# Performance work log

Measured on AMD Instinct MI355X. Metric: run time of the kernel, lower is better.

Reference implementation:

```python
import jax, jax.numpy as jnp
import numpy as np

COMMIT_WEIGHT = 0.25


def setup_inputs() -> dict:
    key = jax.random.key(0)
    k1, k2 = jax.random.split(key)
    B, D, T, K = 8, 512, 2048, 8192
    x = jax.random.normal(k1, (B, D, T), dtype=jnp.float32)
    codebook = jax.random.normal(k2, (K, D), dtype=jnp.float32)
    return {"x": x, "codebook": codebook}


def reference(x, codebook):
    # x: [B, D, T] channels-first; VQ operates on [B, T, D]
    xt = jnp.transpose(x, (0, 2, 1))  # [B, T, D]
    x2 = jnp.sum(xt * xt, axis=-1, keepdims=True)          # [B, T, 1]
    e2 = jnp.sum(codebook * codebook, axis=-1)             # [K]
    xe = jnp.einsum('btd,kd->btk', xt, codebook)           # [B, T, K] (dominant GEMM)
    dists = x2 - 2.0 * xe + e2                             # [B, T, K]
    indices = jnp.argmin(dists, axis=-1)                   # [B, T] int
    quantized = codebook[indices]                          # [B, T, D] gather
    # commitment loss: ||sg(q) - x||^2 mean
    commit_loss = COMMIT_WEIGHT * jnp.mean(
        (jax.lax.stop_gradient(quantized) - xt) ** 2)
    # straight-through estimator
    quantized = xt + jax.lax.stop_gradient(quantized - xt)
    quantized = jnp.transpose(quantized, (0, 2, 1))        # back to [B, D, T]
    return quantized, indices, commit_loss
```

## Files before the change

kernel.cpp:

```cpp
#include <hip/hip_runtime.h>
#include <cstdint>
#include <cstddef>

#define B_   8
#define D_   512
#define T_   2048
#define K_   8192
#define BT_  (B_ * T_)
#define NQ_  ((size_t)B_ * D_ * T_)

typedef _Float16 f16x8 __attribute__((ext_vector_type(8)));
typedef _Float16 f16x4 __attribute__((ext_vector_type(4)));
typedef float    f32x4 __attribute__((ext_vector_type(4)));
typedef unsigned long long u64;
typedef unsigned int u32;

#define WS_SLOTS_OFF    0
#define WS_FIDX_OFF     393216
#define WS_PART_OFF     458752
#define WS_E2_OFF       460800
#define WS_XH_OFF       524288
#define WS_XL_OFF       (WS_XH_OFF + 16777216)
#define WS_CH_OFF       (WS_XL_OFF + 16777216)
#define WS_NEEDED       ((size_t)WS_CH_OFF + 8388608)

__device__ __forceinline__ void gload_lds16(const void* g, void* l) {
    __builtin_amdgcn_global_load_lds(
        (const __attribute__((address_space(1))) void*)g,
        (__attribute__((address_space(3))) void*)l, 16, 0, 0);
}

__device__ __forceinline__ u32 fkey(float f) {
    u32 u = __float_as_uint(f);
    u ^= (u32)((int)u >> 31) | 0x80000000u;
    return u;
}
__device__ __forceinline__ u64 umin64(u64 a, u64 b) { return a < b ? a : b; }
__device__ __forceinline__ u64 umax64(u64 a, u64 b) { return a > b ? a : b; }

__global__ __launch_bounds__(256) void k_e2(const float* __restrict__ cb,
                                            float* __restrict__ e2) {
    int k = blockIdx.x * 256 + threadIdx.x;
    const float4* row = (const float4*)(cb + (size_t)k * D_);
    float s = 0.f;
#pragma unroll 4
    for (int i = 0; i < D_ / 4; ++i) {
        float4 v = row[i];
        s = fmaf(v.x, v.x, s); s = fmaf(v.y, v.y, s);
        s = fmaf(v.z, v.z, s); s = fmaf(v.w, v.w, s);
    }
    e2[k] = s;
}

__global__ __launch_bounds__(256) void k_splitcb(const float* __restrict__ cb,
                                                 _Float16* __restrict__ ch) {
    size_t i = ((size_t)blockIdx.x * 256 + threadIdx.x) * 4;
    float4 v = *(const float4*)(cb + i);
    f16x4 h;
    h[0] = (_Float16)v.x; h[1] = (_Float16)v.y;
    h[2] = (_Float16)v.z; h[3] = (_Float16)v.w;
    *(f16x4*)(ch + i) = h;
}

__global__ __launch_bounds__(256) void k_splitx(const float* __restrict__ x,
                                                _Float16* __restrict__ xh,
                                                _Float16* __restrict__ xl) {
    int b  = blockIdx.z;
    int d0 = blockIdx.y * 64;
    int t0 = blockIdx.x * 64;
    int dl = threadIdx.x & 63;
    int tq = threadIdx.x >> 6;
    const float* px = x + ((size_t)b * D_ + (d0 + dl)) * T_ + t0;
#pragma unroll 4
    for (int i = 0; i < 16; ++i) {
        int t = tq * 16 + i;
        float v = px[t];
        _Float16 h = (_Float16)v;
        float lo = v - (float)h;
        _Float16 l = (_Float16)lo;
        size_t row = (size_t)b * T_ + t0 + t;
        xh[row * D_ + d0 + dl] = h;
        xl[row * D_ + d0 + dl] = l;
    }
}

__global__ __launch_bounds__(256, 2)
void k_hi_argmin(const _Float16* __restrict__ xh, const _Float16* __restrict__ ch,
                 const float* __restrict__ e2, u64* __restrict__ slots) {
    __shared__ char smem[65536];
    __shared__ u32 stop[128][2][2];
    __shared__ float e2s[1024];

    const int tid = threadIdx.x;
    const int xcd = blockIdx.x & 7;
    const int bi  = blockIdx.x >> 3;
    const int m_  = bi >> 3;
    const int nblk = bi & 7;
    const int mbase  = (xcd * 16 + m_) * 128;
    const int nstart = nblk * 1024;

    const int lane = tid & 63;
    const int wid  = tid >> 6;
    const int wr = wid >> 1, wc = wid & 1;
    const int lr = lane & 15, lg = lane >> 4;

    {
        u32* p = (u32*)stop;
        p[tid] = ~0u; p[tid + 256] = ~0u;
        *(float4*)&e2s[tid * 4] = *(const float4*)&e2[nstart + tid * 4];
    }
    __syncthreads();

    const bool isA = wid < 2;
    const int half = wid & 1;
    const int srow8 = lane >> 3;
    const int sswz = ((lane & 7) ^ srow8) * 16;
    const char* gs0 = isA
        ? (const char*)xh + (size_t)(mbase  + half * 64 + srow8) * 1024 + sswz
        : (const char*)ch + (size_t)(nstart + half * 64 + srow8) * 1024 + sswz;
    const int ldsbase = (isA ? 0 : 16384) + half * 8192;

#define STAGE(bufi, g) do {                                                  \
        char* lb_ = smem + (bufi) * 32768 + ldsbase;                         \
        const char* gs_ = gs0 + (isA ? 0 : (size_t)((g) >> 3) * 131072)      \
                          + ((g) & 7) * 128;                                 \
        _Pragma("unroll")                                                    \
        for (int i_ = 0; i_ < 8; ++i_)                                       \
            gload_lds16(gs_ + (size_t)i_ * 8192, lb_ + i_ * 1024);           \
    } while (0)

    const int s7 = lr & 7;
    const int aoff0 = (wr * 64 + lr) * 128 + ((lg ^ s7) * 16);
    const int boff0 = 16384 + (wc * 64 + lr) * 128 + ((lg ^ s7) * 16);

    u32 top2a[16], top2b[16];
#pragma unroll
    for (int s = 0; s < 16; ++s) { top2a[s] = ~0u; top2b[s] = ~0u; }

    f32x4 acc[4][4];
#pragma unroll
    for (int m = 0; m < 4; ++m)
#pragma unroll
        for (int n = 0; n < 4; ++n)
            acc[m][n] = (f32x4){0.f, 0.f, 0.f, 0.f};

    auto epilogue = [&](int ns) {
        float e2v[4];
#pragma unroll
        for (int n = 0; n < 4; ++n)
            e2v[n] = 0.5f * e2s[ns * 128 + wc * 64 + n * 16 + lr];
        const u32 base10 = ((u32)ns << 7) | ((u32)wc << 6) | (u32)lr;
#pragma unroll
        for (int m = 0; m < 4; ++m) {
#pragma unroll
            for (int j = 0; j < 4; ++j) {
                const int s = m * 4 + j;
                u32 t1 = top2a[s], t2 = top2b[s];
#pragma unroll
                for (int n = 0; n < 4; ++n) {
                    float d = fmaxf(e2v[n] - acc[m][n][j], 1.0f);
                    u32 p = (__float_as_uint(d) & 0xFFFFFC00u) | (base10 + ((u32)n << 4));
                    u32 mx = t1 > p ? t1 : p;
                    t1 = t1 < p ? t1 : p;
                    t2 = t2 < mx ? t2 : mx;
                }
                top2a[s] = t1; top2b[s] = t2;
            }
        }
#pragma unroll
        for (int m = 0; m < 4; ++m)
#pragma unroll
            for (int n = 0; n < 4; ++n)
                acc[m][n] = (f32x4){0.f, 0.f, 0.f, 0.f};
    };

    STAGE(0, 0);
    int cur = 0;

#pragma unroll 1
    for (int t = 0; t < 64; ++t) {
        if (t < 63) {
            STAGE(cur ^ 1, t + 1);
            asm volatile("s_waitcnt vmcnt(8)" ::: "memory");
        } else {
            asm volatile("s_waitcnt vmcnt(0)" ::: "memory");
        }
        __builtin_amdgcn_s_barrier();
        __builtin_amdgcn_sched_barrier(0);

        const char* base = smem + cur * 32768;
        f16x8 a0, a1, a2, a3, b0, b1, b2, b3;
        f16x8 c0, c1, c2, c3, d0, d1, d2, d3;
        a0 = *(const f16x8*)(base + aoff0);
        a1 = *(const f16x8*)(base + aoff0 + 2048);
        a2 = *(const f16x8*)(base + aoff0 + 4096);
        a3 = *(const f16x8*)(base + aoff0 + 6144);
        b0 = *(const f16x8*)(base + boff0);
        b1 = *(const f16x8*)(base + boff0 + 2048);
        b2 = *(const f16x8*)(base + boff0 + 4096);
        b3 = *(const f16x8*)(base + boff0 + 6144);
        c0 = *(const f16x8*)(base + (aoff0 ^ 64));
        c1 = *(const f16x8*)(base + ((aoff0 + 2048) ^ 64));
        c2 = *(const f16x8*)(base + ((aoff0 + 4096) ^ 64));
        c3 = *(const f16x8*)(base + ((aoff0 + 6144) ^ 64));
        d0 = *(const f16x8*)(base + (boff0 ^ 64));
        d1 = *(const f16x8*)(base + ((boff0 + 2048) ^ 64));
        d2 = *(const f16x8*)(base + ((boff0 + 4096) ^ 64));
        d3 = *(const f16x8*)(base + ((boff0 + 6144) ^ 64));

        __builtin_amdgcn_s_setprio(1);
        acc[0][0] = __builtin_amdgcn_mfma_f32_16x16x32_f16(a0, b0, acc[0][0], 0, 0, 0);
        acc[0][1] = __builtin_amdgcn_mfma_f32_16x16x32_f16(a0, b1, acc[0][1], 0, 0, 0);
        acc[0][2] = __builtin_amdgcn_mfma_f32_16x16x32_f16(a0, b2, acc[0][2], 0, 0, 0);
        acc[0][3] = __builtin_amdgcn_mfma_f32_16x16x32_f16(a0, b3, acc[0][3], 0, 0, 0);
        acc[1][0] = __builtin_amdgcn_mfma_f32_16x16x32_f16(a1, b0, acc[1][0], 0, 0, 0);
        acc[1][1] = __builtin_amdgcn_mfma_f32_16x16x32_f16(a1, b1, acc[1][1], 0, 0, 0);
        acc[1][2] = __builtin_amdgcn_mfma_f32_16x16x32_f16(a1, b2, acc[1][2], 0, 0, 0);
        acc[1][3] = __builtin_amdgcn_mfma_f32_16x16x32_f16(a1, b3, acc[1][3], 0, 0, 0);
        acc[2][0] = __builtin_amdgcn_mfma_f32_16x16x32_f16(a2, b0, acc[2][0], 0, 0, 0);
        acc[2][1] = __builtin_amdgcn_mfma_f32_16x16x32_f16(a2, b1, acc[2][1], 0, 0, 0);
        acc[2][2] = __builtin_amdgcn_mfma_f32_16x16x32_f16(a2, b2, acc[2][2], 0, 0, 0);
        acc[2][3] = __builtin_amdgcn_mfma_f32_16x16x32_f16(a2, b3, acc[2][3], 0, 0, 0);
        acc[3][0] = __builtin_amdgcn_mfma_f32_16x16x32_f16(a3, b0, acc[3][0], 0, 0, 0);
        acc[3][1] = __builtin_amdgcn_mfma_f32_16x16x32_f16(a3, b1, acc[3][1], 0, 0, 0);
        acc[3][2] = __builtin_amdgcn_mfma_f32_16x16x32_f16(a3, b2, acc[3][2], 0, 0, 0);
        acc[3][3] = __builtin_amdgcn_mfma_f32_16x16x32_f16(a3, b3, acc[3][3], 0, 0, 0);
        acc[0][0] = __builtin_amdgcn_mfma_f32_16x16x32_f16(c0, d0, acc[0][0], 0, 0, 0);
        acc[0][1] = __builtin_amdgcn_mfma_f32_16x16x32_f16(c0, d1, acc[0][1], 0, 0, 0);
        acc[0][2] = __builtin_amdgcn_mfma_f32_16x16x32_f16(c0, d2, acc[0][2], 0, 0, 0);
        acc[0][3] = __builtin_amdgcn_mfma_f32_16x16x32_f16(c0, d3, acc[0][3], 0, 0, 0);
        acc[1][0] = __builtin_amdgcn_mfma_f32_16x16x32_f16(c1, d0, acc[1][0], 0, 0, 0);
        acc[1][1] = __builtin_amdgcn_mfma_f32_16x16x32_f16(c1, d1, acc[1][1], 0, 0, 0);
        acc[1][2] = __builtin_amdgcn_mfma_f32_16x16x32_f16(c1, d2, acc[1][2], 0, 0, 0);
        acc[1][3] = __builtin_amdgcn_mfma_f32_16x16x32_f16(c1, d3, acc[1][3], 0, 0, 0);
        acc[2][0] = __builtin_amdgcn_mfma_f32_16x16x32_f16(c2, d0, acc[2][0], 0, 0, 0);
        acc[2][1] = __builtin_amdgcn_mfma_f32_16x16x32_f16(c2, d1, acc[2][1], 0, 0, 0);
        acc[2][2] = __builtin_amdgcn_mfma_f32_16x16x32_f16(c2, d2, acc[2][2], 0, 0, 0);
        acc[2][3] = __builtin_amdgcn_mfma_f32_16x16x32_f16(c2, d3, acc[2][3], 0, 0, 0);
        acc[3][0] = __builtin_amdgcn_mfma_f32_16x16x32_f16(c3, d0, acc[3][0], 0, 0, 0);
        acc[3][1] = __builtin_amdgcn_mfma_f32_16x16x32_f16(c3, d1, acc[3][1], 0, 0, 0);
        acc[3][2] = __builtin_amdgcn_mfma_f32_16x16x32_f16(c3, d2, acc[3][2], 0, 0, 0);
        acc[3][3] = __builtin_amdgcn_mfma_f32_16x16x32_f16(c3, d3, acc[3][3], 0, 0, 0);
        __builtin_amdgcn_s_setprio(0);

        __builtin_amdgcn_sched_barrier(0);
        __builtin_amdgcn_s_barrier();
        cur ^= 1;
        if ((t & 7) == 7) epilogue(t >> 3);
    }
#undef STAGE

#pragma unroll
    for (int m = 0; m < 4; ++m) {
#pragma unroll
        for (int j = 0; j < 4; ++j) {
            const int s = m * 4 + j;
            u32 t1 = top2a[s], t2 = top2b[s];
#pragma unroll
            for (int st = 1; st < 16; st <<= 1) {
                u32 o1 = __shfl_xor(t1, st);
                u32 o2 = __shfl_xor(t2, st);
                u32 mx = t1 > o1 ? t1 : o1;
                u32 sel = t1 < o1 ? t2 : o2;
                u32 n2 = mx < sel ? mx : sel;
                t1 = t1 < o1 ? t1 : o1;
                t2 = t2 < n2 ? t2 : n2;
            }
            if (lr == 0) {
                int ql = wr * 64 + m * 16 + lg * 4 + j;
                stop[ql][wc][0] = t1; stop[ql][wc][1] = t2;
            }
        }
    }

    __syncthreads();
    if (tid < 128) {
        u32 a1 = stop[tid][0][0], a2 = stop[tid][0][1];
        u32 b1 = stop[tid][1][0], b2 = stop[tid][1][1];
        u32 f1 = a1 < b1 ? a1 : b1;
        u32 mx = a1 > b1 ? a1 : b1;
        u32 sel = a1 < b1 ? a2 : b2;
        u32 f2 = mx < sel ? mx : sel;
        int q = mbase + tid;
        u64 p1 = ((u64)(f1 & 0xFFFFFC00u) << 32) | (u32)(nstart + (f1 & 0x3FFu));
        u64 p2 = ((u64)(f2 & 0xFFFFFC00u) << 32) | (u32)(nstart + (f2 & 0x3FFu));
        u64* As = slots + q;
        u64* Bs = slots + BT_ + q;
        u64* Cs = slots + 2 * BT_ + q;
        u64 old = atomicMin(As, p1);
        u64 v = umax64(old, p1);
        old = atomicMin(Bs, v);
        u64 v2 = umax64(old, v);
        atomicMin(Cs, v2);
        old = atomicMin(Bs, p2);
        v = umax64(old, p2);
        atomicMin(Cs, v);
    }
}

__global__ __launch_bounds__(256)
void k_rescore(const _Float16* __restrict__ xh, const _Float16* __restrict__ xl,
               const float* __restrict__ cb, const float* __restrict__ e2,
               const u64* __restrict__ slots,
               u32* __restrict__ final_idx, float* __restrict__ out_idx) {
    const int wid = threadIdx.x >> 6, lane = threadIdx.x & 63;
    const int q = blockIdx.x * 4 + wid;
    u64 a = slots[q], b = slots[BT_ + q], c = slots[2 * BT_ + q];
    u32 i1 = (u32)a, i2 = (u32)b, i3 = (u32)c;
    float d1 = __uint_as_float((u32)(a >> 32));
    float d2 = __uint_as_float((u32)(b >> 32));
    u32 win = i1;
    if (!(d2 - d1 > 0.75f)) {
        float xr[8];
        f16x8 hv = *(const f16x8*)(xh + (size_t)q * D_ + lane * 8);
        f16x8 lv = *(const f16x8*)(xl + (size_t)q * D_ + lane * 8);
#pragma unroll
        for (int i = 0; i < 8; ++i) xr[i] = (float)hv[i] + (float)lv[i];
        u32 idxs[3] = {i1, i2, i3};
        float key[3];
#pragma unroll 1
        for (int cnd = 0; cnd < 3; ++cnd) {
            const float4* cr = (const float4*)(cb + (size_t)idxs[cnd] * D_ + lane * 8);
            float4 c0 = cr[0], c1 = cr[1];
            float s = xr[0] * c0.x;
            s = fmaf(xr[1], c0.y, s); s = fmaf(xr[2], c0.z, s); s = fmaf(xr[3], c0.w, s);
            s = fmaf(xr[4], c1.x, s); s = fmaf(xr[5], c1.y, s);
            s = fmaf(xr[6], c1.z, s); s = fmaf(xr[7], c1.w, s);
#pragma unroll
            for (int st = 1; st < 64; st <<= 1) s += __shfl_xor(s, st);
            key[cnd] = e2[idxs[cnd]] - 2.f * s;
        }
        float bk = key[0]; win = idxs[0];
#pragma unroll
        for (int cnd = 1; cnd < 3; ++cnd) {
            if (key[cnd] < bk || (key[cnd] == bk && idxs[cnd] < win)) {
                bk = key[cnd]; win = idxs[cnd];
            }
        }
    }
    if (lane == 0) { final_idx[q] = win; out_idx[q] = (float)win; }
}

#define MB 64
#define NB 64
#define KC 32
#define FNSPLIT 2
#define KPER (K_ / FNSPLIT)
__global__ __launch_bounds__(256, 2)
void k_argmin_f32(const float* __restrict__ x, const float* __restrict__ cb,
                  const float* __restrict__ e2, u64* __restrict__ slots) {
    __shared__ float xs[KC][MB + 4];
    __shared__ float es[KC][NB + 4];
    __shared__ u64 red[MB];
    const int tid = threadIdx.x;
    const int tx = tid & 15, ty = tid >> 4;
    const int rowtile = blockIdx.x;
    const int b = rowtile >> 5;
    const int tbase = (rowtile & 31) * MB;
    const int nstart = blockIdx.y * KPER;
    if (tid < MB) red[tid] = ~0ull;
    float bestv[4]; int besti[4];
#pragma unroll
    for (int i = 0; i < 4; ++i) { bestv[i] = 3.4e38f; besti[i] = 0; }
    const int sm = tid & 63, sg = tid >> 6;
    const float* xbase = x + (size_t)b * D_ * T_ + (tbase + sm);
    for (int nb = 0; nb < KPER; nb += NB) {
        float acc[4][4];
#pragma unroll
        for (int i = 0; i < 4; ++i)
#pragma unroll
            for (int j = 0; j < 4; ++j) acc[i][j] = 0.f;
        for (int kc = 0; kc < D_; kc += KC) {
            __syncthreads();
#pragma unroll
            for (int r = 0; r < 8; ++r) {
                int dd = sg * 8 + r;
                xs[dd][sm] = xbase[(size_t)(kc + dd) * T_];
            }
            const float* crow = cb + (size_t)(nstart + nb + sm) * D_ + kc + sg * 8;
            float4 c0 = *(const float4*)(crow);
            float4 c1 = *(const float4*)(crow + 4);
            es[sg * 8 + 0][sm] = c0.x; es[sg * 8 + 1][sm] = c0.y;
            es[sg * 8 + 2][sm] = c0.z; es[sg * 8 + 3][sm] = c0.w;
            es[sg * 8 + 4][sm] = c1.x; es[sg * 8 + 5][sm] = c1.y;
            es[sg * 8 + 6][sm] = c1.z; es[sg * 8 + 7][sm] = c1.w;
            __syncthreads();
#pragma unroll
            for (int dd = 0; dd < KC; ++dd) {
                float4 a = *(const float4*)&xs[dd][tx * 4];
                float4 e = *(const float4*)&es[dd][ty * 4];
                acc[0][0] = fmaf(a.x, e.x, acc[0][0]); acc[0][1] = fmaf(a.x, e.y, acc[0][1]);
                acc[0][2] = fmaf(a.x, e.z, acc[0][2]); acc[0][3] = fmaf(a.x, e.w, acc[0][3]);
                acc[1][0] = fmaf(a.y, e.x, acc[1][0]); acc[1][1] = fmaf(a.y, e.y, acc[1][1]);
                acc[1][2] = fmaf(a.y, e.z, acc[1][2]); acc[1][3] = fmaf(a.y, e.w, acc[1][3]);
                acc[2][0] = fmaf(a.z, e.x, acc[2][0]); acc[2][1] = fmaf(a.z, e.y, acc[2][1]);
                acc[2][2] = fmaf(a.z, e.z, acc[2][2]); acc[2][3] = fmaf(a.z, e.w, acc[2][3]);
                acc[3][0] = fmaf(a.w, e.x, acc[3][0]); acc[3][1] = fmaf(a.w, e.y, acc[3][1]);
                acc[3][2] = fmaf(a.w, e.z, acc[3][2]); acc[3][3] = fmaf(a.w, e.w, acc[3][3]);
            }
        }
#pragma unroll
        for (int j = 0; j < 4; ++j) {
            int c = nstart + nb + ty * 4 + j;
            float ec = e2[c];
#pragma unroll
            for (int i = 0; i < 4; ++i) {
                float dist = fmaf(-2.f, acc[i][j], ec);
                if (dist < bestv[i]) { bestv[i] = dist; besti[i] = c; }
            }
        }
    }
    __syncthreads();
#pragma unroll
    for (int i = 0; i < 4; ++i) {
        u64 p = ((u64)fkey(bestv[i]) << 32) | (u32)besti[i];
        atomicMin(&red[tx * 4 + i], p);
    }
    __syncthreads();
    if (tid < MB) atomicMin(&slots[b * T_ + tbase + tid], red[tid]);
}

__global__ __launch_bounds__(256)
void k_finalize(const u64* __restrict__ slots,
                u32* __restrict__ final_idx, float* __restrict__ out_idx) {
    int q = blockIdx.x * 256 + threadIdx.x;
    u32 idx = (u32)slots[q];
    final_idx[q] = idx;
    out_idx[q] = (float)idx;
}

__global__ __launch_bounds__(256)
void k_gather(const float* __restrict__ x, const float* __restrict__ cb,
              const u32* __restrict__ final_idx,
              float* __restrict__ out_q, float* __restrict__ partials) {
    int tid = threadIdx.x;
    int btg = blockIdx.x * 256 + tid;
    int b = btg >> 11, t = btg & (T_ - 1);
    int dch = blockIdx.y;
    u32 idx = final_idx[btg];
    const float* crow = cb + (size_t)idx * D_;
    size_t xoff = (size_t)b * D_ * T_ + t;
    float ls = 0.f;
#pragma unroll 4
    for (int dd = 0; dd < 64; ++dd) {
        int d = dch * 64 + dd;
        float q = crow[d];
        size_t o = xoff + (size_t)d * T_;
        float xv = x[o];
        out_q[o] = q;
        float df = q - xv;
        ls = fmaf(df, df, ls);
    }
    __shared__ float rs[256];
    rs[tid] = ls;
    __syncthreads();
    for (int s = 128; s > 0; s >>= 1) {
        if (tid < s) rs[tid] += rs[tid + s];
        __syncthreads();
    }
    if (tid == 0) partials[blockIdx.y * 64 + blockIdx.x] = rs[0];
}

__global__ __launch_bounds__(256)
void k_loss(const float* __restrict__ partials, float* __restrict__ out_loss) {
    __shared__ float rs[256];
    int tid = threadIdx.x;
    float s = partials[tid] + partials[tid + 256];
    rs[tid] = s;
    __syncthreads();
    for (int st = 128; st > 0; st >>= 1) {
        if (tid < st) rs[tid] += rs[tid + st];
        __syncthreads();
    }
    if (tid == 0) out_loss[0] = 0.25f * rs[0] / (float)NQ_;
}

extern "C" void kernel_launch(void* const* d_in, const int* in_sizes, int n_in,
                              void* d_out, int out_size, void* d_ws, size_t ws_size,
                              hipStream_t stream) {
    const float* x  = (const float*)d_in[0];
    const float* cb = (const float*)d_in[1];

    float* out_q    = (float*)d_out;
    float* out_idx  = out_q + NQ_;
    float* out_loss = out_idx + BT_;

    char* ws = (char*)d_ws;
    u64* slots = (u64*)(ws + WS_SLOTS_OFF);
    u32* fidx = (u32*)(ws + WS_FIDX_OFF);
    float* partials = (float*)(ws + WS_PART_OFF);
    float* e2 = (float*)(ws + WS_E2_OFF);

    hipMemsetAsync(slots, 0xFF, (size_t)3 * BT_ * 8, stream);
    k_e2<<<dim3(K_ / 256), dim3(256), 0, stream>>>(cb, e2);

    if (ws_size >= WS_NEEDED) {
        _Float16* xhp = (_Float16*)(ws + WS_XH_OFF);
        _Float16* xlp = (_Float16*)(ws + WS_XL_OFF);
        _Float16* chp = (_Float16*)(ws + WS_CH_OFF);
        k_splitcb<<<dim3((K_ * D_ / 4) / 256), dim3(256), 0, stream>>>(cb, chp);
        k_splitx<<<dim3(T_ / 64, D_ / 64, B_), dim3(256), 0, stream>>>(x, xhp, xlp);
        k_hi_argmin<<<dim3(1024), dim3(256), 0, stream>>>(xhp, chp, e2, slots);
        k_rescore<<<dim3(BT_ / 4), dim3(256), 0, stream>>>(xhp, xlp, cb, e2, slots,
                                                           fidx, out_idx);
    } else {
        k_argmin_f32<<<dim3(BT_ / MB, FNSPLIT), dim3(256), 0, stream>>>(x, cb, e2, slots);
        k_finalize<<<dim3(BT_ / 256), dim3(256), 0, stream>>>(slots, fidx, out_idx);
    }

    k_gather<<<dim3(BT_ / 256, D_ / 64), dim3(256), 0, stream>>>(x, cb, fidx,
                                                                 out_q, partials);
    k_loss<<<dim3(1), dim3(256), 0, stream>>>(partials, out_loss);
}
```

Baseline: 234.6 us.

## Enlarge argmin GEMM tile to 256x256 with 8 waves and phased MFMA schedule

Doubles the k_hi_argmin block to 512 threads, each computing a 256x256 tile (4x8 MFMA tiles per wave) over 32 K-steps of 64, with 128KB of double-buffered LDS. The inner loop is restructured into four phases of LDS fragment loads and MFMA bursts separated by barriers, with global prefetch issued early. This aims to raise arithmetic intensity and cut global/LDS traffic per flop, but it doubles accumulator registers and LDS use, which risks lower occupancy, register spills, and more barrier overhead.

```diff
diff --git a/kernel.cpp b/kernel.cpp
--- a/kernel.cpp
+++ b/kernel.cpp
@@ -84,11 +84,11 @@
     }
 }
 
-__global__ __launch_bounds__(256, 2)
+__global__ __launch_bounds__(512, 2)
 void k_hi_argmin(const _Float16* __restrict__ xh, const _Float16* __restrict__ ch,
                  const float* __restrict__ e2, u64* __restrict__ slots) {
-    __shared__ char smem[65536];
-    __shared__ u32 stop[128][2][2];
+    __shared__ char smem[131072];
+    __shared__ u32 stop[256][2][2];
     __shared__ float e2s[1024];
 
     const int tid = threadIdx.x;
@@ -96,33 +96,32 @@
     const int bi  = blockIdx.x >> 3;
     const int m_  = bi >> 3;
     const int nblk = bi & 7;
-    const int mbase  = (xcd * 16 + m_) * 128;
+    const int mbase  = (xcd * 8 + m_) * 256;
     const int nstart = nblk * 1024;
 
     const int lane = tid & 63;
     const int wid  = tid >> 6;
-    const int wr = wid >> 1, wc = wid & 1;
+    const int wr = wid & 3, wc = wid >> 2;
     const int lr = lane & 15, lg = lane >> 4;
 
     {
         u32* p = (u32*)stop;
-        p[tid] = ~0u; p[tid + 256] = ~0u;
-        *(float4*)&e2s[tid * 4] = *(const float4*)&e2[nstart + tid * 4];
+        p[tid] = ~0u; p[tid + 512] = ~0u;
+        *(float2*)&e2s[tid * 2] = *(const float2*)&e2[nstart + tid * 2];
     }
     __syncthreads();
 
-    const bool isA = wid < 2;
-    const int half = wid & 1;
+    const bool isA = wid < 4;
     const int srow8 = lane >> 3;
     const int sswz = ((lane & 7) ^ srow8) * 16;
     const char* gs0 = isA
-        ? (const char*)xh + (size_t)(mbase  + half * 64 + srow8) * 1024 + sswz
-        : (const char*)ch + (size_t)(nstart + half * 64 + srow8) * 1024 + sswz;
-    const int ldsbase = (isA ? 0 : 16384) + half * 8192;
+        ? (const char*)xh + (size_t)(mbase  + (wid & 3) * 64 + srow8) * 1024 + sswz
+        : (const char*)ch + (size_t)(nstart + (wid & 3) * 64 + srow8) * 1024 + sswz;
+    const int ldsbase = (isA ? 0 : 32768) + (wid & 3) * 8192;
 
 #define STAGE(bufi, g) do {                                                  \
-        char* lb_ = smem + (bufi) * 32768 + ldsbase;                         \
-        const char* gs_ = gs0 + (isA ? 0 : (size_t)((g) >> 3) * 131072)      \
+        char* lb_ = smem + (bufi) * 65536 + ldsbase;                         \
+        const char* gs_ = gs0 + (isA ? 0 : (size_t)((g) >> 3) * 262144)      \
                           + ((g) & 7) * 128;                                 \
         _Pragma("unroll")                                                    \
         for (int i_ = 0; i_ < 8; ++i_)                                       \
@@ -131,25 +130,25 @@
 
     const int s7 = lr & 7;
     const int aoff0 = (wr * 64 + lr) * 128 + ((lg ^ s7) * 16);
-    const int boff0 = 16384 + (wc * 64 + lr) * 128 + ((lg ^ s7) * 16);
+    const int boff0 = 32768 + (wc * 128 + lr) * 128 + ((lg ^ s7) * 16);
 
     u32 top2a[16], top2b[16];
 #pragma unroll
     for (int s = 0; s < 16; ++s) { top2a[s] = ~0u; top2b[s] = ~0u; }
 
-    f32x4 acc[4][4];
+    f32x4 acc[4][8];
 #pragma unroll
     for (int m = 0; m < 4; ++m)
 #pragma unroll
-        for (int n = 0; n < 4; ++n)
+        for (int n = 0; n < 8; ++n)
             acc[m][n] = (f32x4){0.f, 0.f, 0.f, 0.f};
 
     auto epilogue = [&](int ns) {
-        float e2v[4];
-#pragma unroll
-        for (int n = 0; n < 4; ++n)
-            e2v[n] = 0.5f * e2s[ns * 128 + wc * 64 + n * 16 + lr];
-        const u32 base10 = ((u32)ns << 7) | ((u32)wc << 6) | (u32)lr;
+        float e2v[8];
+#pragma unroll
+        for (int n = 0; n < 8; ++n)
+            e2v[n] = 0.5f * e2s[ns * 256 + wc * 128 + n * 16 + lr];
+        const u32 base10 = ((u32)ns << 8) | ((u32)wc << 7) | (u32)lr;
 #pragma unroll
         for (int m = 0; m < 4; ++m) {
 #pragma unroll
@@ -157,7 +156,7 @@
                 const int s = m * 4 + j;
                 u32 t1 = top2a[s], t2 = top2b[s];
 #pragma unroll
-                for (int n = 0; n < 4; ++n) {
+                for (int n = 0; n < 8; ++n) {
                     float d = fmaxf(e2v[n] - acc[m][n][j], 1.0f);
                     u32 p = (__float_as_uint(d) & 0xFFFFFC00u) | (base10 + ((u32)n << 4));
                     u32 mx = t1 > p ? t1 : p;
@@ -170,85 +169,83 @@
 #pragma unroll
         for (int m = 0; m < 4; ++m)
 #pragma unroll
-            for (int n = 0; n < 4; ++n)
+            for (int n = 0; n < 8; ++n)
                 acc[m][n] = (f32x4){0.f, 0.f, 0.f, 0.f};
     };
 
+#define MFMA_BLOCK(NOFF)                                                     \
+        __builtin_amdgcn_s_setprio(1);                                       \
+        _Pragma("unroll")                                                    \
+        for (int m = 0; m < 4; ++m)                                          \
+            _Pragma("unroll")                                                \
+            for (int n = 0; n < 4; ++n)                                      \
+                acc[m][(NOFF) + n] = __builtin_amdgcn_mfma_f32_16x16x32_f16( \
+                    af[m], bf[n], acc[m][(NOFF) + n], 0, 0, 0);              \
+        __builtin_amdgcn_s_setprio(0);
+
     STAGE(0, 0);
+    asm volatile("s_waitcnt vmcnt(0)" ::: "memory");
+    __builtin_amdgcn_s_barrier();
     int cur = 0;
 
 #pragma unroll 1
-    for (int t = 0; t < 64; ++t) {
-        if (t < 63) {
-            STAGE(cur ^ 1, t + 1);
-            asm volatile("s_waitcnt vmcnt(8)" ::: "memory");
-        } else {
-            asm volatile("s_waitcnt vmcnt(0)" ::: "memory");
-        }
-        __builtin_amdgcn_s_barrier();
-        __builtin_amdgcn_sched_barrier(0);
-
-        const char* base = smem + cur * 32768;
-        f16x8 a0, a1, a2, a3, b0, b1, b2, b3;
-        f16x8 c0, c1, c2, c3, d0, d1, d2, d3;
-        a0 = *(const f16x8*)(base + aoff0);
-        a1 = *(const f16x8*)(base + aoff0 + 2048);
-        a2 = *(const f16x8*)(base + aoff0 + 4096);
-        a3 = *(const f16x8*)(base + aoff0 + 6144);
-        b0 = *(const f16x8*)(base + boff0);
-        b1 = *(const f16x8*)(base + boff0 + 2048);
-        b2 = *(const f16x8*)(base + boff0 + 4096);
-        b3 = *(const f16x8*)(base + boff0 + 6144);
-        c0 = *(const f16x8*)(base + (aoff0 ^ 64));
-        c1 = *(const f16x8*)(base + ((aoff0 + 2048) ^ 64));
-        c2 = *(const f16x8*)(base + ((aoff0 + 4096) ^ 64));
-        c3 = *(const f16x8*)(base + ((aoff0 + 6144) ^ 64));
-        d0 = *(const f16x8*)(base + (boff0 ^ 64));
-        d1 = *(const f16x8*)(base + ((boff0 + 2048) ^ 64));
-        d2 = *(const f16x8*)(base + ((boff0 + 4096) ^ 64));
-        d3 = *(const f16x8*)(base + ((boff0 + 6144) ^ 64));
-
-        __builtin_amdgcn_s_setprio(1);
-        acc[0][0] = __builtin_amdgcn_mfma_f32_16x16x32_f16(a0, b0, acc[0][0], 0, 0, 0);
-        acc[0][1] = __builtin_amdgcn_mfma_f32_16x16x32_f16(a0, b1, acc[0][1], 0, 0, 0);
-        acc[0][2] = __builtin_amdgcn_mfma_f32_16x16x32_f16(a0, b2, acc[0][2], 0, 0, 0);
-        acc[0][3] = __builtin_amdgcn_mfma_f32_16x16x32_f16(a0, b3, acc[0][3], 0, 0, 0);
-        acc[1][0] = __builtin_amdgcn_mfma_f32_16x16x32_f16(a1, b0, acc[1][0], 0, 0, 0);
-        acc[1][1] = __builtin_amdgcn_mfma_f32_16x16x32_f16(a1, b1, acc[1][1], 0, 0, 0);
-        acc[1][2] = __builtin_amdgcn_mfma_f32_16x16x32_f16(a1, b2, acc[1][2], 0, 0, 0);
-        acc[1][3] = __builtin_amdgcn_mfma_f32_16x16x32_f16(a1, b3, acc[1][3], 0, 0, 0);
-        acc[2][0] = __builtin_amdgcn_mfma_f32_16x16x32_f16(a2, b0, acc[2][0], 0, 0, 0);
-        acc[2][1] = __builtin_amdgcn_mfma_f32_16x16x32_f16(a2, b1, acc[2][1], 0, 0, 0);
-        acc[2][2] = __builtin_amdgcn_mfma_f32_16x16x32_f16(a2, b2, acc[2][2], 0, 0, 0);
-        acc[2][3] = __builtin_amdgcn_mfma_f32_16x16x32_f16(a2, b3, acc[2][3], 0, 0, 0);
-        acc[3][0] = __builtin_amdgcn_mfma_f32_16x16x32_f16(a3, b0, acc[3][0], 0, 0, 0);
-        acc[3][1] = __builtin_amdgcn_mfma_f32_16x16x32_f16(a3, b1, acc[3][1], 0, 0, 0);
-        acc[3][2] = __builtin_amdgcn_mfma_f32_16x16x32_f16(a3, b2, acc[3][2], 0, 0, 0);
-        acc[3][3] = __builtin_amdgcn_mfma_f32_16x16x32_f16(a3, b3, acc[3][3], 0, 0, 0);
-        acc[0][0] = __builtin_amdgcn_mfma_f32_16x16x32_f16(c0, d0, acc[0][0], 0, 0, 0);
-        acc[0][1] = __builtin_amdgcn_mfma_f32_16x16x32_f16(c0, d1, acc[0][1], 0, 0, 0);
-        acc[0][2] = __builtin_amdgcn_mfma_f32_16x16x32_f16(c0, d2, acc[0][2], 0, 0, 0);
-        acc[0][3] = __builtin_amdgcn_mfma_f32_16x16x32_f16(c0, d3, acc[0][3], 0, 0, 0);
-        acc[1][0] = __builtin_amdgcn_mfma_f32_16x16x32_f16(c1, d0, acc[1][0], 0, 0, 0);
-        acc[1][1] = __builtin_amdgcn_mfma_f32_16x16x32_f16(c1, d1, acc[1][1], 0, 0, 0);
-        acc[1][2] = __builtin_amdgcn_mfma_f32_16x16x32_f16(c1, d2, acc[1][2], 0, 0, 0);
-        acc[1][3] = __builtin_amdgcn_mfma_f32_16x16x32_f16(c1, d3, acc[1][3], 0, 0, 0);
-        acc[2][0] = __builtin_amdgcn_mfma_f32_16x16x32_f16(c2, d0, acc[2][0], 0, 0, 0);
-        acc[2][1] = __builtin_amdgcn_mfma_f32_16x16x32_f16(c2, d1, acc[2][1], 0, 0, 0);
-        acc[2][2] = __builtin_amdgcn_mfma_f32_16x16x32_f16(c2, d2, acc[2][2], 0, 0, 0);
-        acc[2][3] = __builtin_amdgcn_mfma_f32_16x16x32_f16(c2, d3, acc[2][3], 0, 0, 0);
-        acc[3][0] = __builtin_amdgcn_mfma_f32_16x16x32_f16(c3, d0, acc[3][0], 0, 0, 0);
-        acc[3][1] = __builtin_amdgcn_mfma_f32_16x16x32_f16(c3, d1, acc[3][1], 0, 0, 0);
-        acc[3][2] = __builtin_amdgcn_mfma_f32_16x16x32_f16(c3, d2, acc[3][2], 0, 0, 0);
-        acc[3][3] = __builtin_amdgcn_mfma_f32_16x16x32_f16(c3, d3, acc[3][3], 0, 0, 0);
-        __builtin_amdgcn_s_setprio(0);
-
-        __builtin_amdgcn_sched_barrier(0);
-        __builtin_amdgcn_s_barrier();
+    for (int t = 0; t < 32; ++t) {
+        const char* base = smem + cur * 65536;
+        f16x8 af[4], bf[4];
+
+#pragma unroll
+        for (int m = 0; m < 4; ++m)
+            af[m] = *(const f16x8*)(base + aoff0 + m * 2048);
+#pragma unroll
+        for (int n = 0; n < 4; ++n)
+            bf[n] = *(const f16x8*)(base + boff0 + n * 2048);
+        __builtin_amdgcn_sched_barrier(0);
+        if (t < 31) STAGE(cur ^ 1, t + 1);
+        __builtin_amdgcn_s_barrier();
+        __builtin_amdgcn_sched_barrier(0);
+        MFMA_BLOCK(0)
+        __builtin_amdgcn_sched_barrier(0);
+        __builtin_amdgcn_s_barrier();
+
+#pragma unroll
+        for (int n = 0; n < 4; ++n)
+            bf[n] = *(const f16x8*)(base + boff0 + (4 + n) * 2048);
+        __builtin_amdgcn_sched_barrier(0);
+        __builtin_amdgcn_s_barrier();
+        __builtin_amdgcn_sched_barrier(0);
+        MFMA_BLOCK(4)
+        __builtin_amdgcn_sched_barrier(0);
+        __builtin_amdgcn_s_barrier();
+
+#pragma unroll
+        for (int m = 0; m < 4; ++m)
+            af[m] = *(const f16x8*)(base + (aoff0 ^ 64) + m * 2048);
+#pragma unroll
+        for (int n = 0; n < 4; ++n)
+            bf[n] = *(const f16x8*)(base + (boff0 ^ 64) + n * 2048);
+        __builtin_amdgcn_sched_barrier(0);
+        __builtin_amdgcn_s_barrier();
+        __builtin_amdgcn_sched_barrier(0);
+        MFMA_BLOCK(0)
+        __builtin_amdgcn_sched_barrier(0);
+        __builtin_amdgcn_s_barrier();
+
+#pragma unroll
+        for (int n = 0; n < 4; ++n)
+            bf[n] = *(const f16x8*)(base + (boff0 ^ 64) + (4 + n) * 2048);
+        __builtin_amdgcn_sched_barrier(0);
+        asm volatile("s_waitcnt vmcnt(0)" ::: "memory");
+        __builtin_amdgcn_s_barrier();
+        __builtin_amdgcn_sched_barrier(0);
+        MFMA_BLOCK(4)
+        __builtin_amdgcn_sched_barrier(0);
+        __builtin_amdgcn_s_barrier();
+
         cur ^= 1;
         if ((t & 7) == 7) epilogue(t >> 3);
     }
 #undef STAGE
+#undef MFMA_BLOCK
 
 #pragma unroll
     for (int m = 0; m < 4; ++m) {
@@ -274,7 +271,7 @@
     }
 
     __syncthreads();
-    if (tid < 128) {
+    if (tid < 256) {
         u32 a1 = stop[tid][0][0], a2 = stop[tid][0][1];
         u32 b1 = stop[tid][1][0], b2 = stop[tid][1][1];
         u32 f1 = a1 < b1 ? a1 : b1;
@@ -500,7 +497,7 @@
         _Float16* chp = (_Float16*)(ws + WS_CH_OFF);
         k_splitcb<<<dim3((K_ * D_ / 4) / 256), dim3(256), 0, stream>>>(cb, chp);
         k_splitx<<<dim3(T_ / 64, D_ / 64, B_), dim3(256), 0, stream>>>(x, xhp, xlp);
-        k_hi_argmin<<<dim3(1024), dim3(256), 0, stream>>>(xhp, chp, e2, slots);
+        k_hi_argmin<<<dim3(512), dim3(512), 0, stream>>>(xhp, chp, e2, slots);
         k_rescore<<<dim3(BT_ / 4), dim3(256), 0, stream>>>(xhp, xlp, cb, e2, slots,
                                                            fidx, out_idx);
     } else {
```

Result: faster. 218.3 us (-6.9%).
